# Performance work log

Measured on AMD Instinct MI355X. Metric: run time of the kernel, lower is better.

## Reference

```python
import jax, jax.numpy as jnp
import numpy as np

B, L, C = 4, 2048, 2048
NH, HD, K = 32, 64, 16  # num_heads, head_dim, inner chunk size
LR = 1.0
EPS = 1e-6


def ln_fwd(x, w, b):
    # F.layer_norm over last dim (biased variance), eps=1e-6
    mu = x.mean(-1, keepdims=True)
    var = x.var(-1, keepdims=True)
    xhat = (x - mu) * jax.lax.rsqrt(var + EPS)
    return w * xhat + b


def ln_fused_l2_bwd(x, target, w, b):
    # grad wrt x of 0.5*||LN(x;w,b) - target||^2 fused with LN fwd
    D = x.shape[-1]
    mu = x.mean(-1, keepdims=True)
    var = x.var(-1, keepdims=True)
    std = jnp.sqrt(var + EPS)
    xhat = (x - mu) / std
    y = w * xhat + b
    g = (y - target) * w  # dL/d(xhat)
    return (D * g - g.sum(-1, keepdims=True) - xhat * (g * xhat).sum(-1, keepdims=True)) / (D * std)


def _inner_scan(XC, XB, XA, coeff, W1, b1, lnw, lnb):
    # per (batch, head): XC/XB/XA [n_chunk,K,HD], coeff [n_chunk,K,1], W1 [HD,HD], b1 [1,HD], lnw/lnb [HD]
    mask = jnp.tril(jnp.ones((K, K), XC.dtype))

    def step(carry, inp):
        W1c, b1c = carry
        xc, xb, xa, co = inp
        Z1 = xb @ W1c + b1c                       # [K,HD]
        grad = ln_fused_l2_bwd(Z1, xa - xb, lnw, lnb)
        Attn1 = mask * (xc @ xb.T)                # [K,K] causal
        b1_bar = b1c - (co * mask) @ grad         # [K,HD]
        Z1_bar = xc @ W1c - (co * Attn1) @ grad + b1_bar
        W1n = W1c - (co[-1] * xb).T @ grad        # fast-weight update with last coeff
        b1n = b1_bar[-1:]
        out = xc + ln_fwd(Z1_bar, lnw, lnb)       # post-LN residual
        return (W1n, b1n), out

    _, ys = jax.lax.scan(step, (W1, b1), (XC, XB, XA, coeff))
    return ys.reshape(-1, HD)  # [L,HD]


def setup_inputs() -> dict:
    key = jax.random.key(0)
    ks = jax.random.split(key, 9)
    s = 0.02
    return {
        'hidden_states': jax.random.normal(ks[0], (B, L, C), jnp.float32),
        'Wq': jax.random.normal(ks[1], (C, NH * HD), jnp.float32) * s,
        'Wk': jax.random.normal(ks[2], (C, NH * HD), jnp.float32) * s,
        'Wv': jax.random.normal(ks[3], (C, NH * HD), jnp.float32) * s,
        'Wo': jax.random.normal(ks[4], (NH * HD, C), jnp.float32) * s,
        'ilr_w': jax.random.normal(ks[5], (C, NH), jnp.float32) * s,
        'ilr_b': jnp.zeros((NH,), jnp.float32),
        'ln_weight': jnp.ones((NH, HD), jnp.float32),
        'ln_bias': jnp.zeros((NH, HD), jnp.float32),
        'W1': jax.random.normal(ks[6], (NH, HD, HD), jnp.float32) * s,
        'b1': jnp.zeros((NH, 1, HD), jnp.float32),
    }


def reference(hidden_states, Wq, Wk, Wv, Wo, ilr_w, ilr_b, ln_weight, ln_bias, W1, b1):
    n_chunk = L // K

    def split(x):  # [B,L,NH*HD] -> [B,NH,n_chunk,K,HD]
        return x.reshape(B, n_chunk, K, NH, HD).transpose(0, 3, 1, 2, 4)

    XC = split(hidden_states @ Wq)
    XB = split(hidden_states @ Wk)
    XA = split(hidden_states @ Wv)

    # sigmoid-gated per-token learning rates
    ilr = jax.nn.sigmoid(hidden_states @ ilr_w + ilr_b)          # [B,L,NH]
    ilr = ilr.reshape(B, n_chunk, K, NH).transpose(0, 3, 1, 2)[..., None]  # [B,NH,n_chunk,K,1]
    token_idx = 1.0 / jnp.arange(1, K + 1, dtype=jnp.float32)
    coeff = (LR * token_idx).reshape(1, 1, 1, K, 1) * ilr / HD

    per_head = jax.vmap(_inner_scan, in_axes=(0, 0, 0, 0, 0, 0, 0, 0))
    per_batch = jax.vmap(per_head, in_axes=(0, 0, 0, 0, None, None, None, None))
    XCW = per_batch(XC, XB, XA, coeff, W1, b1, ln_weight, ln_bias)  # [B,NH,L,HD]
    XCW = XCW.transpose(0, 2, 1, 3).reshape(B, L, NH * HD)
    return XCW @ Wo
```

## Files before the change

### kernel.cpp

```cpp
#include <hip/hip_runtime.h>
#include <hip/hip_bf16.h>

typedef __attribute__((ext_vector_type(8))) short bf16x8;
typedef __attribute__((ext_vector_type(4))) short bf16x4;
typedef __attribute__((ext_vector_type(4))) float f32x4;
typedef __attribute__((ext_vector_type(8))) unsigned short u16x8;
typedef unsigned short u16;

#define AS1(p) ((__attribute__((address_space(1))) void*)(p))
#define AS3(p) ((__attribute__((address_space(3))) void*)(p))
#define GLL16(g, l) __builtin_amdgcn_global_load_lds(AS1(g), AS3(l), 16, 0, 0)

__device__ __forceinline__ u16 f2bf(float x) {
  return __builtin_bit_cast(u16, __float2bfloat16(x));
}
__device__ __forceinline__ float bf2f(u16 u) {
  return __builtin_bit_cast(float, ((unsigned)u) << 16);
}
__device__ __forceinline__ f32x4 mfma16(bf16x8 a, bf16x8 b, f32x4 c) {
  return __builtin_amdgcn_mfma_f32_16x16x32_bf16(a, b, c, 0, 0, 0);
}
__device__ __forceinline__ f32x4 mfma16k(bf16x4 a, bf16x4 b, f32x4 c) {
#if defined(__HIP_DEVICE_COMPILE__)
#if __has_builtin(__builtin_amdgcn_mfma_f32_16x16x16bf16_1k)
  return __builtin_amdgcn_mfma_f32_16x16x16bf16_1k(a, b, c, 0, 0, 0);
#else
  f32x4 d;
  asm volatile("v_mfma_f32_16x16x16_bf16 %0, %1, %2, %3"
               : "=v"(d)
               : "v"(a), "v"(b), "v"(c));
  return d;
#endif
#else
  (void)a; (void)b;
  return c;
#endif
}
#define DPPADD(x, ctrl)                                                            \
  ((x) + __builtin_bit_cast(float, __builtin_amdgcn_update_dpp(                    \
             0, __builtin_bit_cast(int, (x)), (ctrl), 0xf, 0xf, true)))
__device__ __forceinline__ float rsum16(float x) {
  x = DPPADD(x, 0x128);
  x = DPPADD(x, 0x124);
  x = DPPADD(x, 0x122);
  x = DPPADD(x, 0x121);
  return x;
}

__global__ __launch_bounds__(256) void conv_bf16(const float* __restrict__ in,
                                                 u16* __restrict__ out) {
  size_t g = (size_t)blockIdx.x * 256 + threadIdx.x;
  const float4* p = reinterpret_cast<const float4*>(in) + g * 2;
  float4 a = p[0], b = p[1];
  u16x8 r;
  r[0] = f2bf(a.x); r[1] = f2bf(a.y); r[2] = f2bf(a.z); r[3] = f2bf(a.w);
  r[4] = f2bf(b.x); r[5] = f2bf(b.y); r[6] = f2bf(b.z); r[7] = f2bf(b.w);
  *reinterpret_cast<u16x8*>(out + g * 8) = r;
}

__global__ __launch_bounds__(256) void wt_conv(const float* __restrict__ W,
                                               u16* __restrict__ Wt, int Kd, int N) {
  __shared__ float t[64][65];
  const int n0 = blockIdx.x * 64, k0 = blockIdx.y * 64;
  const int tx = threadIdx.x & 63, ty = threadIdx.x >> 6;
#pragma unroll
  for (int rr = 0; rr < 16; ++rr) {
    int r = rr * 4 + ty;
    t[r][tx] = W[(size_t)(k0 + r) * N + n0 + tx];
  }
  __syncthreads();
#pragma unroll
  for (int rr = 0; rr < 16; ++rr) {
    int r = rr * 4 + ty;
    Wt[(size_t)(n0 + r) * Kd + k0 + tx] = f2bf(t[tx][r]);
  }
}

__global__ __launch_bounds__(256) void ilr_strip(const float* __restrict__ ilr_w,
                                                 u16* __restrict__ WcatT) {
  int g = blockIdx.x * 256 + threadIdx.x;
  int p = g >> 11, k = g & 2047;
  float v = (p < 32) ? ilr_w[k * 32 + p] : 0.f;
  WcatT[(size_t)(6144 + p) * 2048 + k] = f2bf(v);
}

__device__ __forceinline__ void stage_pair(const u16* __restrict__ A, const u16* __restrict__ Bt,
                                           u16* As, u16* Bs, int Kd, int mT, int nT, int kt,
                                           int tid) {
#pragma unroll
  for (int r = 0; r < 2; ++r) {
    int e = r * 2048 + tid * 8;
    int row = e >> 5, kk = e & 31;
    GLL16(A + (size_t)(mT + row) * Kd + kt + kk, As + e);
    GLL16(Bt + (size_t)(nT + row) * Kd + kt + kk, Bs + e);
  }
}

template <int MODE>
__global__ __launch_bounds__(256) void gemm_bt(const u16* __restrict__ A,
                                               const u16* __restrict__ Bt, int M, int N, int Kd,
                                               u16* __restrict__ O0, u16* __restrict__ O1,
                                               u16* __restrict__ O2,
                                               float* __restrict__ coeffOut,
                                               const float* __restrict__ ilrb,
                                               float* __restrict__ Cout) {
  __shared__ __align__(16) u16 As[2][4096];
  __shared__ __align__(16) u16 Bs[2][4096];
  const int tid = threadIdx.x;
  const int lane = tid & 63;
  const int wid = tid >> 6;
  const int wr = wid >> 1, wc = wid & 1;
  const int l15 = lane & 15, l4 = lane >> 4;
  const int mT = blockIdx.y << 7, nT = blockIdx.x << 7;

  f32x4 acc[4][4];
#pragma unroll
  for (int m = 0; m < 4; ++m)
#pragma unroll
    for (int n = 0; n < 4; ++n) acc[m][n] = (f32x4){0.f, 0.f, 0.f, 0.f};

  stage_pair(A, Bt, &As[0][0], &Bs[0][0], Kd, mT, nT, 0, tid);
  const int nIter = Kd >> 5;
  const int aoff = (wr * 64 + l15) * 32 + l4 * 8;
  const int boff = (wc * 64 + l15) * 32 + l4 * 8;
#pragma unroll 1
  for (int it = 0; it < nIter; ++it) {
    const int cur = it & 1;
    __syncthreads();
    if (it + 1 < nIter)
      stage_pair(A, Bt, &As[cur ^ 1][0], &Bs[cur ^ 1][0], Kd, mT, nT, (it + 1) << 5, tid);
    bf16x8 av[4], bv[4];
#pragma unroll
    for (int x = 0; x < 4; ++x) {
      av[x] = *reinterpret_cast<const bf16x8*>(&As[cur][aoff + x * 512]);
      bv[x] = *reinterpret_cast<const bf16x8*>(&Bs[cur][boff + x * 512]);
    }
#pragma unroll
    for (int m = 0; m < 4; ++m)
#pragma unroll
      for (int n = 0; n < 4; ++n) acc[m][n] = mfma16(av[m], bv[n], acc[m][n]);
  }
#pragma unroll
  for (int m = 0; m < 4; ++m) {
#pragma unroll
    for (int n = 0; n < 4; ++n) {
      const int col = nT + wc * 64 + n * 16 + l15;
#pragma unroll
      for (int e = 0; e < 4; ++e) {
        const int row = mT + wr * 64 + m * 16 + l4 * 4 + e;
        float v = acc[m][n][e];
        if constexpr (MODE == 1) {
          Cout[(size_t)row * N + col] = v;
        } else {
          const int bb = row >> 11, lt = row & 2047;
          if (col < 6144) {
            const int mat = col >> 11;
            u16* base = (mat == 0) ? O0 : ((mat == 1) ? O1 : O2);
            const int hh = (col >> 6) & 31, dd = col & 63;
            base[(((size_t)(bb * 32 + hh)) * 2048 + lt) * 64 + dd] = f2bf(v);
          } else {
            const int h3 = col - 6144;
            if (h3 < 32) {
              const float x = v + ilrb[h3];
              const float sig = 1.f / (1.f + expf(-x));
              const int tok = lt & 15;
              coeffOut[((size_t)(bb * 32 + h3)) * 2048 + lt] =
                  sig * (1.f / (64.f * (float)(tok + 1)));
            }
          }
        }
      }
    }
  }
  (void)M;
}

__global__ __launch_bounds__(64) void ttt_scan(
    const u16* __restrict__ XC, const u16* __restrict__ XB, const u16* __restrict__ XA,
    const float* __restrict__ coeff, const float* __restrict__ lnw_g,
    const float* __restrict__ lnb_g, const float* __restrict__ W1g,
    const float* __restrict__ b1g, u16* __restrict__ XCW) {
  const int bh = blockIdx.x;
  const int b = bh >> 5, h = bh & 31;
  const int lane = threadIdx.x & 63;
  const int l15 = lane & 15, l4 = lane >> 4;

  const u16* xbb = XB + (size_t)bh * 131072;
  const u16* xcb = XC + (size_t)bh * 131072;
  const u16* xab = XA + (size_t)bh * 131072;
  const float* cob = coeff + (size_t)bh * 2048;

  float lnw4[4], lnb4[4], b1m[4];
#pragma unroll
  for (int cb = 0; cb < 4; ++cb) {
    lnw4[cb] = lnw_g[h * 64 + cb * 16 + l15];
    lnb4[cb] = lnb_g[h * 64 + cb * 16 + l15];
    b1m[cb] = b1g[h * 64 + cb * 16 + l15];
  }
  f32x4 mW[4][4];
#pragma unroll
  for (int kb = 0; kb < 4; ++kb)
#pragma unroll
    for (int cb = 0; cb < 4; ++cb)
#pragma unroll
      for (int e = 0; e < 4; ++e)
        mW[kb][cb][e] = W1g[(size_t)h * 4096 + (kb * 16 + l4 * 4 + e) * 64 + cb * 16 + l15];

  uint2 nxbA[4], nxcA[4];
  float nco[4], nco15, ncoL;
  const int foA = l15 * 128 + l4 * 8;
#define PF(cc)                                                                       \
  do {                                                                               \
    const char* pb = (const char*)(xbb + (cc) * 1024);                               \
    const char* pc = (const char*)(xcb + (cc) * 1024);                               \
    _Pragma("unroll") for (int kb = 0; kb < 4; ++kb) {                               \
      nxbA[kb] = *(const uint2*)(pb + foA + kb * 32);                                \
      nxcA[kb] = *(const uint2*)(pc + foA + kb * 32);                                \
    }                                                                                \
    _Pragma("unroll") for (int e = 0; e < 4; ++e) nco[e] = cob[(cc) * 16 + l4 * 4 + e]; \
    nco15 = cob[(cc) * 16 + 15];                                                     \
    ncoL = cob[(cc) * 16 + l15];                                                     \
  } while (0)

  PF(0);

#pragma unroll 1
  for (int c = 0; c < 128; ++c) {
    bf16x4 xbA[4], xcA[4];
#pragma unroll
    for (int kb = 0; kb < 4; ++kb) {
      xbA[kb] = __builtin_bit_cast(bf16x4, nxbA[kb]);
      xcA[kb] = __builtin_bit_cast(bf16x4, nxcA[kb]);
    }
    float co_own[4];
#pragma unroll
    for (int e = 0; e < 4; ++e) co_own[e] = nco[e];
    const float co15 = nco15, coL = ncoL;

    u16 sxa[4][4], sxb[4][4], sxc[4][4];
    {
      const u16* xap_ = xab + c * 1024;
      const u16* xbp_ = xbb + c * 1024;
      const u16* xcp_ = xcb + c * 1024;
#pragma unroll
      for (int cb = 0; cb < 4; ++cb)
#pragma unroll
        for (int e = 0; e < 4; ++e) {
          const int idx = (l4 * 4 + e) * 64 + cb * 16 + l15;
          sxa[cb][e] = xap_[idx];
          sxb[cb][e] = xbp_[idx];
          sxc[cb][e] = xcp_[idx];
        }
    }
    PF((c < 127) ? (c + 1) : 127);

    f32x4 pT = {0.f, 0.f, 0.f, 0.f};
#pragma unroll
    for (int kb = 0; kb < 4; ++kb) pT = mfma16k(xbA[kb], xcA[kb], pT);
    bf16x4 pTf;
#pragma unroll
    for (int e = 0; e < 4; ++e) {
      const int r = l4 * 4 + e;
      pTf[e] = (short)f2bf((r <= l15) ? pT[e] * (-coL) : 0.f);
    }

    bf16x4 w1b[4][4];
#pragma unroll
    for (int kb = 0; kb < 4; ++kb)
#pragma unroll
      for (int cb = 0; cb < 4; ++cb)
#pragma unroll
        for (int e = 0; e < 4; ++e) w1b[kb][cb][e] = (short)f2bf(mW[kb][cb][e]);

    f32x4 z[4], o2[4];
#pragma unroll
    for (int cb = 0; cb < 4; ++cb) {
      f32x4 a = {b1m[cb], b1m[cb], b1m[cb], b1m[cb]};
#pragma unroll
      for (int kb = 0; kb < 4; ++kb) a = mfma16k(xbA[kb], w1b[kb][cb], a);
      z[cb] = a;
      f32x4 a2 = {0.f, 0.f, 0.f, 0.f};
#pragma unroll
      for (int kb = 0; kb < 4; ++kb) a2 = mfma16k(xcA[kb], w1b[kb][cb], a2);
      o2[cb] = a2;
    }

    float gr[4][4];
#pragma unroll
    for (int e = 0; e < 4; ++e) {
      float zz[4];
#pragma unroll
      for (int cb = 0; cb < 4; ++cb) zz[cb] = z[cb][e];
      float s1 = zz[0] + zz[1] + zz[2] + zz[3];
      float s2 = zz[0] * zz[0] + zz[1] * zz[1] + zz[2] * zz[2] + zz[3] * zz[3];
      s1 = rsum16(s1);
      s2 = rsum16(s2);
      const float mu = s1 * 0.015625f;
      const float var = fmaxf(s2 * 0.015625f - mu * mu, 0.f);
      const float rstd = rsqrtf(var + 1e-6f);
      float xh[4], gl[4];
#pragma unroll
      for (int cb = 0; cb < 4; ++cb) {
        xh[cb] = (zz[cb] - mu) * rstd;
        const float tgt = bf2f(sxa[cb][e]) - bf2f(sxb[cb][e]);
        gl[cb] = (fmaf(lnw4[cb], xh[cb], lnb4[cb]) - tgt) * lnw4[cb];
      }
      float gs = gl[0] + gl[1] + gl[2] + gl[3];
      float gx = gl[0] * xh[0] + gl[1] * xh[1] + gl[2] * xh[2] + gl[3] * xh[3];
      gs = rsum16(gs);
      gx = rsum16(gx);
#pragma unroll
      for (int cb = 0; cb < 4; ++cb)
        gr[cb][e] = (64.f * gl[cb] - gs - xh[cb] * gx) * (rstd * 0.015625f);
    }

    float gtot[4], lower[4];
#pragma unroll
    for (int cb = 0; cb < 4; ++cb) {
      const float T = gr[cb][0] + gr[cb][1] + gr[cb][2] + gr[cb][3];
      const float t1 = __shfl_xor(T, 16, 64);
      const float t2 = __shfl_xor(T, 32, 64);
      const float t3 = __shfl_xor(t1, 32, 64);
      gtot[cb] = T + t1 + t2 + t3;
      lower[cb] = ((l4 & 1) ? t1 : 0.f) + ((l4 & 2) ? (t2 + t3) : 0.f);
    }

    bf16x4 grB[4];
#pragma unroll
    for (int cb = 0; cb < 4; ++cb)
#pragma unroll
      for (int e = 0; e < 4; ++e) grB[cb][e] = (short)f2bf(gr[cb][e]);

#pragma unroll
    for (int cb = 0; cb < 4; ++cb) o2[cb] = mfma16k(pTf, grB[cb], o2[cb]);

    bf16x4 xbU[4];
#pragma unroll
    for (int kb = 0; kb < 4; ++kb)
#pragma unroll
      for (int e = 0; e < 4; ++e)
        xbU[kb][e] = (short)f2bf(bf2f(sxb[kb][e]) * (-co15));
#pragma unroll
    for (int kb = 0; kb < 4; ++kb)
#pragma unroll
      for (int cb = 0; cb < 4; ++cb) mW[kb][cb] = mfma16k(xbU[kb], grB[cb], mW[kb][cb]);

    float ov[4][4];
#pragma unroll
    for (int cb = 0; cb < 4; ++cb) {
      float pfx = lower[cb];
#pragma unroll
      for (int e = 0; e < 4; ++e) {
        pfx += gr[cb][e];
        ov[cb][e] = o2[cb][e] + fmaf(-co_own[e], pfx, b1m[cb]);
      }
    }
#pragma unroll
    for (int e = 0; e < 4; ++e) {
      float s1 = ov[0][e] + ov[1][e] + ov[2][e] + ov[3][e];
      float s2 = ov[0][e] * ov[0][e] + ov[1][e] * ov[1][e] + ov[2][e] * ov[2][e] +
                 ov[3][e] * ov[3][e];
      s1 = rsum16(s1);
      s2 = rsum16(s2);
      const float mu = s1 * 0.015625f;
      const float var = fmaxf(s2 * 0.015625f - mu * mu, 0.f);
      const float rstd = rsqrtf(var + 1e-6f);
      const size_t rowg = (size_t)(b * 2048 + c * 16 + l4 * 4 + e) * 2048 + h * 64;
#pragma unroll
      for (int cb = 0; cb < 4; ++cb) {
        const float y = bf2f(sxc[cb][e]) + fmaf(lnw4[cb], (ov[cb][e] - mu) * rstd, lnb4[cb]);
        XCW[rowg + cb * 16 + l15] = f2bf(y);
      }
    }

#pragma unroll
    for (int cb = 0; cb < 4; ++cb) b1m[cb] = fmaf(-co15, gtot[cb], b1m[cb]);
  }
#undef PF
}

extern "C" void kernel_launch(void* const* d_in, const int* in_sizes, int n_in, void* d_out,
                              int out_size, void* d_ws, size_t ws_size, hipStream_t stream) {
  const float* hs = (const float*)d_in[0];
  const float* Wq = (const float*)d_in[1];
  const float* Wk = (const float*)d_in[2];
  const float* Wv = (const float*)d_in[3];
  const float* Wo = (const float*)d_in[4];
  const float* ilr_w = (const float*)d_in[5];
  const float* ilr_b = (const float*)d_in[6];
  const float* lnw = (const float*)d_in[7];
  const float* lnb = (const float*)d_in[8];
  const float* W1 = (const float*)d_in[9];
  const float* b1 = (const float*)d_in[10];
  float* out = (float*)d_out;

  if (ws_size < 93847552u) return;
  char* ws = (char*)d_ws;
  u16* hsb = (u16*)(ws + 0);
  u16* WcatT = (u16*)(ws + 33554432);
  u16* XCbf = (u16*)(ws + 59244544);
  float* coeffb = (float*)(ws + 92798976);
  u16* XCW = hsb;
  u16* WoT = (u16*)(ws + 33554432);
  u16* XBbf = (u16*)d_out;
  u16* XAbf = (u16*)((char*)d_out + 33554432);

  conv_bf16<<<8192, 256, 0, stream>>>(hs, hsb);
  wt_conv<<<dim3(32, 32), 256, 0, stream>>>(Wq, WcatT, 2048, 2048);
  wt_conv<<<dim3(32, 32), 256, 0, stream>>>(Wk, WcatT + (size_t)2048 * 2048, 2048, 2048);
  wt_conv<<<dim3(32, 32), 256, 0, stream>>>(Wv, WcatT + (size_t)4096 * 2048, 2048, 2048);
  ilr_strip<<<1024, 256, 0, stream>>>(ilr_w, WcatT);

  gemm_bt<0><<<dim3(49, 64), 256, 0, stream>>>(hsb, WcatT, 8192, 6272, 2048, XCbf, XBbf, XAbf,
                                               coeffb, ilr_b, nullptr);
  wt_conv<<<dim3(32, 32), 256, 0, stream>>>(Wo, WoT, 2048, 2048);
  ttt_scan<<<128, 64, 0, stream>>>(XCbf, XBbf, XAbf, coeffb, lnw, lnb, W1, b1, XCW);
  gemm_bt<1><<<dim3(16, 64), 256, 0, stream>>>(XCW, WoT, 8192, 2048, 2048, nullptr, nullptr,
                                               nullptr, nullptr, nullptr, out);

  (void)in_sizes; (void)n_in; (void)out_size;
}
```

Measured before the change: 715.9 us.

## Replace 128x128 GEMM with 256x256 8-wave pipelined kernel using swizzled LDS

Swaps the simple double-buffered 128x128x32 bf16 GEMM for a 512-thread 256x256x64 kernel with XOR-swizzled LDS, split staging of A/B halves interleaved with MFMA quadrants, explicit waitcnt/barriers and setprio. This targets the two projection GEMMs, aiming for higher arithmetic intensity, fewer bank conflicts and better overlap of global loads with MFMA. It raises register and LDS pressure (128KB LDS). The 6272-wide N now yields a partial last tile that is guarded on loads but relies on the epilogue's column check.

```diff
diff --git a/kernel.cpp b/kernel.cpp
--- a/kernel.cpp
+++ b/kernel.cpp
@@ -84,71 +84,158 @@
   WcatT[(size_t)(6144 + p) * 2048 + k] = f2bf(v);
 }
 
-__device__ __forceinline__ void stage_pair(const u16* __restrict__ A, const u16* __restrict__ Bt,
-                                           u16* As, u16* Bs, int Kd, int mT, int nT, int kt,
-                                           int tid) {
-#pragma unroll
-  for (int r = 0; r < 2; ++r) {
-    int e = r * 2048 + tid * 8;
-    int row = e >> 5, kk = e & 31;
-    GLL16(A + (size_t)(mT + row) * Kd + kt + kk, As + e);
-    GLL16(Bt + (size_t)(nT + row) * Kd + kt + kk, Bs + e);
+template <int MODE>
+__global__ __launch_bounds__(512) void gemm8p(const u16* __restrict__ A,
+                                              const u16* __restrict__ Bt, int M, int N, int Kd,
+                                              u16* __restrict__ O0, u16* __restrict__ O1,
+                                              u16* __restrict__ O2,
+                                              float* __restrict__ coeffOut,
+                                              const float* __restrict__ ilrb,
+                                              float* __restrict__ Cout) {
+  __shared__ __align__(16) u16 Asm[2][2][8192];
+  __shared__ __align__(16) u16 Bsm[2][2][8192];
+  const int tid = threadIdx.x;
+  const int lane = tid & 63, wid = tid >> 6;
+  const int wr = wid >> 2, wc = wid & 3;
+  const int l15 = lane & 15, l4 = lane >> 4;
+  const int wc1 = wc & 1, wch = wc >> 1;
+  const int swzm = (l15 & 3) ^ (((l15 >> 2) & 1) << 2);
+  const int mT = blockIdx.y << 8, nT = blockIdx.x << 8;
+  const int nKt = Kd >> 6;
+
+#define STG_A(kt_, h_)                                                              \
+  do {                                                                              \
+    if ((kt_) < nKt) {                                                              \
+      _Pragma("unroll") for (int i_ = 0; i_ < 2; ++i_) {                            \
+        const int s_ = tid + 512 * i_;                                              \
+        const int r_ = s_ >> 3;                                                     \
+        const int sc_ = (s_ & 7) ^ (r_ & 3) ^ (((r_ >> 2) & 1) << 2);               \
+        GLL16(A + (size_t)(mT + (h_) * 128 + r_) * Kd + (kt_) * 64 + sc_ * 8,       \
+              &Asm[(kt_) & 1][h_][0] + s_ * 8);                                     \
+      }                                                                             \
+    }                                                                               \
+  } while (0)
+#define STG_B(kt_, h_)                                                              \
+  do {                                                                              \
+    if ((kt_) < nKt) {                                                              \
+      _Pragma("unroll") for (int i_ = 0; i_ < 2; ++i_) {                            \
+        const int s_ = tid + 512 * i_;                                              \
+        const int r_ = s_ >> 3;                                                     \
+        const int sc_ = (s_ & 7) ^ (r_ & 3) ^ (((r_ >> 2) & 1) << 2);               \
+        const int rg_ = nT + (h_) * 128 + r_;                                       \
+        if (rg_ < N)                                                                \
+          GLL16(Bt + (size_t)rg_ * Kd + (kt_) * 64 + sc_ * 8,                       \
+                &Bsm[(kt_) & 1][h_][0] + s_ * 8);                                   \
+      }                                                                             \
+    }                                                                               \
+  } while (0)
+#define RD_A(buf_, mi_, ks_)                                                        \
+  (*(const bf16x8*)((const char*)&Asm[buf_][wr][0] + 128 * ((mi_) * 16 + l15) +     \
+                    16 * ((l4 + 4 * (ks_)) ^ swzm)))
+#define RD_B(buf_, ni_, ks_)                                                        \
+  (*(const bf16x8*)((const char*)&Bsm[buf_][wch][0] +                               \
+                    128 * (wc1 * 64 + (ni_) * 16 + l15) +                           \
+                    16 * ((l4 + 4 * (ks_)) ^ swzm)))
+#define BARRIER __builtin_amdgcn_s_barrier()
+#define LGKM0                                                                       \
+  do {                                                                              \
+    asm volatile("s_waitcnt lgkmcnt(0)" ::: "memory");                              \
+    __builtin_amdgcn_sched_barrier(0);                                              \
+  } while (0)
+#define VM4 asm volatile("s_waitcnt vmcnt(4)" ::: "memory")
+#define PRIO1 __builtin_amdgcn_s_setprio(1)
+#define PRIO0 __builtin_amdgcn_s_setprio(0)
+#define QUAD(mh_, nh_)                                                              \
+  _Pragma("unroll") for (int m4_ = 0; m4_ < 4; ++m4_)                               \
+  _Pragma("unroll") for (int n2_ = 0; n2_ < 2; ++n2_)                               \
+  _Pragma("unroll") for (int ks_ = 0; ks_ < 2; ++ks_)                               \
+      acc[(mh_) * 4 + m4_][(nh_) * 2 + n2_] =                                       \
+          mfma16(Af[(mh_) * 4 + m4_][ks_], Bf[(nh_) * 2 + n2_][ks_],                \
+                 acc[(mh_) * 4 + m4_][(nh_) * 2 + n2_])
+
+  f32x4 acc[8][4];
+#pragma unroll
+  for (int m = 0; m < 8; ++m)
+#pragma unroll
+    for (int n = 0; n < 4; ++n) acc[m][n] = (f32x4){0.f, 0.f, 0.f, 0.f};
+  bf16x8 Af[8][2], Bf[4][2];
+
+  STG_A(0, 0); STG_A(0, 1); STG_B(0, 0); STG_B(0, 1); STG_A(1, 0); STG_A(1, 1);
+  VM4;
+  BARRIER;
+
+#pragma unroll 1
+  for (int it = 0; it < (nKt >> 1); ++it) {
+    const int T = 2 * it;
+#pragma unroll
+    for (int mi = 0; mi < 4; ++mi)
+#pragma unroll
+      for (int ks = 0; ks < 2; ++ks) Af[mi][ks] = RD_A(0, mi, ks);
+#pragma unroll
+    for (int ni = 0; ni < 2; ++ni)
+#pragma unroll
+      for (int ks = 0; ks < 2; ++ks) Bf[ni][ks] = RD_B(0, ni, ks);
+    STG_B(T + 1, 0);
+    BARRIER; LGKM0; PRIO1; QUAD(0, 0); PRIO0;
+    BARRIER;
+#pragma unroll
+    for (int mi = 4; mi < 8; ++mi)
+#pragma unroll
+      for (int ks = 0; ks < 2; ++ks) Af[mi][ks] = RD_A(0, mi, ks);
+    STG_B(T + 1, 1);
+    BARRIER; LGKM0; PRIO1; QUAD(1, 0); PRIO0;
+    BARRIER;
+#pragma unroll
+    for (int ni = 2; ni < 4; ++ni)
+#pragma unroll
+      for (int ks = 0; ks < 2; ++ks) Bf[ni][ks] = RD_B(0, ni, ks);
+    STG_A(T + 2, 0);
+    BARRIER; LGKM0; PRIO1; QUAD(0, 1); PRIO0;
+    BARRIER;
+    STG_A(T + 2, 1);
+    BARRIER; LGKM0; PRIO1; QUAD(1, 1); PRIO0;
+    VM4;
+    BARRIER;
+#pragma unroll
+    for (int mi = 0; mi < 4; ++mi)
+#pragma unroll
+      for (int ks = 0; ks < 2; ++ks) Af[mi][ks] = RD_A(1, mi, ks);
+#pragma unroll
+    for (int ni = 0; ni < 2; ++ni)
+#pragma unroll
+      for (int ks = 0; ks < 2; ++ks) Bf[ni][ks] = RD_B(1, ni, ks);
+    STG_B(T + 2, 0);
+    BARRIER; LGKM0; PRIO1; QUAD(0, 0); PRIO0;
+    BARRIER;
+#pragma unroll
+    for (int mi = 4; mi < 8; ++mi)
+#pragma unroll
+      for (int ks = 0; ks < 2; ++ks) Af[mi][ks] = RD_A(1, mi, ks);
+    STG_B(T + 2, 1);
+    BARRIER; LGKM0; PRIO1; QUAD(1, 0); PRIO0;
+    BARRIER;
+#pragma unroll
+    for (int ni = 2; ni < 4; ++ni)
+#pragma unroll
+      for (int ks = 0; ks < 2; ++ks) Bf[ni][ks] = RD_B(1, ni, ks);
+    STG_A(T + 3, 0);
+    BARRIER; LGKM0; PRIO1; QUAD(0, 1); PRIO0;
+    BARRIER;
+    STG_A(T + 3, 1);
+    BARRIER; LGKM0; PRIO1; QUAD(1, 1); PRIO0;
+    VM4;
+    BARRIER;
   }
-}
-
-template <int MODE>
-__global__ __launch_bounds__(256) void gemm_bt(const u16* __restrict__ A,
-                                               const u16* __restrict__ Bt, int M, int N, int Kd,
-                                               u16* __restrict__ O0, u16* __restrict__ O1,
-                                               u16* __restrict__ O2,
-                                               float* __restrict__ coeffOut,
-                                               const float* __restrict__ ilrb,
-                                               float* __restrict__ Cout) {
-  __shared__ __align__(16) u16 As[2][4096];
-  __shared__ __align__(16) u16 Bs[2][4096];
-  const int tid = threadIdx.x;
-  const int lane = tid & 63;
-  const int wid = tid >> 6;
-  const int wr = wid >> 1, wc = wid & 1;
-  const int l15 = lane & 15, l4 = lane >> 4;
-  const int mT = blockIdx.y << 7, nT = blockIdx.x << 7;
-
-  f32x4 acc[4][4];
-#pragma unroll
-  for (int m = 0; m < 4; ++m)
-#pragma unroll
-    for (int n = 0; n < 4; ++n) acc[m][n] = (f32x4){0.f, 0.f, 0.f, 0.f};
-
-  stage_pair(A, Bt, &As[0][0], &Bs[0][0], Kd, mT, nT, 0, tid);
-  const int nIter = Kd >> 5;
-  const int aoff = (wr * 64 + l15) * 32 + l4 * 8;
-  const int boff = (wc * 64 + l15) * 32 + l4 * 8;
-#pragma unroll 1
-  for (int it = 0; it < nIter; ++it) {
-    const int cur = it & 1;
-    __syncthreads();
-    if (it + 1 < nIter)
-      stage_pair(A, Bt, &As[cur ^ 1][0], &Bs[cur ^ 1][0], Kd, mT, nT, (it + 1) << 5, tid);
-    bf16x8 av[4], bv[4];
-#pragma unroll
-    for (int x = 0; x < 4; ++x) {
-      av[x] = *reinterpret_cast<const bf16x8*>(&As[cur][aoff + x * 512]);
-      bv[x] = *reinterpret_cast<const bf16x8*>(&Bs[cur][boff + x * 512]);
-    }
-#pragma unroll
-    for (int m = 0; m < 4; ++m)
-#pragma unroll
-      for (int n = 0; n < 4; ++n) acc[m][n] = mfma16(av[m], bv[n], acc[m][n]);
-  }
-#pragma unroll
-  for (int m = 0; m < 4; ++m) {
-#pragma unroll
-    for (int n = 0; n < 4; ++n) {
-      const int col = nT + wc * 64 + n * 16 + l15;
+
+#pragma unroll
+  for (int mi = 0; mi < 8; ++mi) {
+#pragma unroll
+    for (int ni = 0; ni < 4; ++ni) {
+      const int col = nT + wc * 64 + ni * 16 + l15;
 #pragma unroll
       for (int e = 0; e < 4; ++e) {
-        const int row = mT + wr * 64 + m * 16 + l4 * 4 + e;
-        float v = acc[m][n][e];
+        const int row = mT + wr * 128 + mi * 16 + l4 * 4 + e;
+        float v = acc[mi][ni][e];
         if constexpr (MODE == 1) {
           Cout[(size_t)row * N + col] = v;
         } else {
@@ -173,6 +260,11 @@
     }
   }
   (void)M;
+#undef STG_A
+#undef STG_B
+#undef RD_A
+#undef RD_B
+#undef QUAD
 }
 
 __global__ __launch_bounds__(64) void ttt_scan(
@@ -411,12 +503,12 @@
   wt_conv<<<dim3(32, 32), 256, 0, stream>>>(Wv, WcatT + (size_t)4096 * 2048, 2048, 2048);
   ilr_strip<<<1024, 256, 0, stream>>>(ilr_w, WcatT);
 
-  gemm_bt<0><<<dim3(49, 64), 256, 0, stream>>>(hsb, WcatT, 8192, 6272, 2048, XCbf, XBbf, XAbf,
-                                               coeffb, ilr_b, nullptr);
+  gemm8p<0><<<dim3(25, 32), 512, 0, stream>>>(hsb, WcatT, 8192, 6272, 2048, XCbf, XBbf, XAbf,
+                                              coeffb, ilr_b, nullptr);
   wt_conv<<<dim3(32, 32), 256, 0, stream>>>(Wo, WoT, 2048, 2048);
   ttt_scan<<<128, 64, 0, stream>>>(XCbf, XBbf, XAbf, coeffb, lnw, lnb, W1, b1, XCW);
-  gemm_bt<1><<<dim3(16, 64), 256, 0, stream>>>(XCW, WoT, 8192, 2048, 2048, nullptr, nullptr,
-                                               nullptr, nullptr, nullptr, out);
+  gemm8p<1><<<dim3(8, 32), 512, 0, stream>>>(XCW, WoT, 8192, 2048, 2048, nullptr, nullptr,
+                                             nullptr, nullptr, nullptr, out);
 
   (void)in_sizes; (void)n_in; (void)out_size;
 }
```

Result: faster. 650.6 us (-9.1%).
